# Kernel optimization log

Hardware: AMD Instinct MI355X
Metric: run time of the kernel (lower is better)

Reference implementation:

```python
import jax, jax.numpy as jnp
import numpy as np

N, E, F_IN, EF, HID = 100000, 1600000, 32, 8, 16


def gat_conv(x, W, att_src, att_dst, b, src, dst, heads, out_ch):
    # PyG GATConv: h = x@W per head; score = LeakyReLU(a_s.h_src + a_d.h_dst);
    # segment-softmax over incoming edges of each dst; weighted sum of h_src.
    n = x.shape[0]
    h = (x @ W).reshape(n, heads, out_ch)                      # [N,H,C]
    a_s = jnp.sum(h * att_src, axis=-1)                        # [N,H]
    a_d = jnp.sum(h * att_dst, axis=-1)                        # [N,H]
    e = jax.nn.leaky_relu(a_s[src] + a_d[dst], 0.2)            # [E',H]
    m = jax.ops.segment_max(e, dst, num_segments=n)            # [N,H]
    ex = jnp.exp(e - m[dst])
    denom = jax.ops.segment_sum(ex, dst, num_segments=n)
    alpha = ex / (denom[dst] + 1e-16)                          # [E',H]
    out = jax.ops.segment_sum(h[src] * alpha[:, :, None], dst, num_segments=n)
    return out.reshape(n, heads * out_ch) + b


def setup_inputs() -> dict:
    key = jax.random.key(0)
    ks = jax.random.split(key, 16)
    s = 0.1
    return {
        "x": jax.random.normal(ks[0], (N, F_IN), jnp.float32),
        "edge_index": jax.random.randint(ks[1], (2, E), 0, N, jnp.int32),
        "edge_attr": jax.random.uniform(ks[2], (E, 2 * EF), jnp.float32),
        "num_edge_features": EF,
        "num_edge_masks": EF,
        # conv1: heads=4, out=16
        "W1": jax.random.normal(ks[3], (F_IN, 4 * HID), jnp.float32) * s,
        "att_src1": jax.random.normal(ks[4], (4, HID), jnp.float32) * s,
        "att_dst1": jax.random.normal(ks[5], (4, HID), jnp.float32) * s,
        "b1": jnp.zeros((4 * HID,), jnp.float32),
        # conv2: heads=1, out=16
        "W2": jax.random.normal(ks[6], (4 * HID, HID), jnp.float32) * s,
        "att_src2": jax.random.normal(ks[7], (1, HID), jnp.float32) * s,
        "att_dst2": jax.random.normal(ks[8], (1, HID), jnp.float32) * s,
        "b2": jnp.zeros((HID,), jnp.float32),
        # edge MLP
        "mlp_W1": jax.random.normal(ks[9], (EF, HID), jnp.float32) * s,
        "mlp_b1": jnp.zeros((HID,), jnp.float32),
        "mlp_W2": jax.random.normal(ks[10], (HID, HID), jnp.float32) * s,
        "mlp_b2": jnp.zeros((HID,), jnp.float32),
        # fc_edge: 3*hid -> 1
        "fc_W": jax.random.normal(ks[11], (3 * HID, 1), jnp.float32) * s,
        "fc_b": jnp.zeros((1,), jnp.float32),
    }


def reference(x, edge_index, edge_attr, num_edge_features, num_edge_masks,
              W1, att_src1, att_dst1, b1, W2, att_src2, att_dst2, b2,
              mlp_W1, mlp_b1, mlp_W2, mlp_b2, fc_W, fc_b):
    n = x.shape[0]
    src, dst = edge_index[0], edge_index[1]
    # GATConv adds self loops internally (PyG default)
    loops = jnp.arange(n, dtype=edge_index.dtype)
    src_sl = jnp.concatenate([src, loops])
    dst_sl = jnp.concatenate([dst, loops])
    ef = edge_attr[:, :num_edge_features] * edge_attr[:, num_edge_features:]
    h = gat_conv(x, W1, att_src1, att_dst1, b1, src_sl, dst_sl, 4, HID)
    h = jax.nn.elu(h)                                          # dropout: eval mode -> identity
    h = gat_conv(h, W2, att_src2, att_dst2, b2, src_sl, dst_sl, 1, HID)
    ef = jax.nn.relu(ef @ mlp_W1 + mlp_b1) @ mlp_W2 + mlp_b2   # edge MLP
    emb = jnp.concatenate([h[src], h[dst], ef], axis=1)        # [E,3*HID]
    return (emb @ fc_W + fc_b).squeeze(-1)                     # [E]
```

## Files before the change

### kernel.cpp

```cpp
#include <hip/hip_runtime.h>
#include <hip/hip_bf16.h>
#include <hip/hip_fp16.h>


#define FIN 32
#define C1 64
#define HID 16
#define BSH 8
#define CAP2 6144
#define SOP 68
#define BINB 1024
#define BINT 4

__device__ __forceinline__ float leaky02(float x) {
    return x > 0.f ? x : 0.2f * x;
}

__global__ void k_binit3(int* __restrict__ bcur, int nbuck) {
    int b = blockIdx.x * blockDim.x + threadIdx.x;
    if (b < nbuck) bcur[b] = b * CAP2;
}

__global__ void __launch_bounds__(256) k_binF(
        const int* __restrict__ src, const int* __restrict__ dst,
        int* __restrict__ bcur, unsigned* __restrict__ brec,
        const float* __restrict__ ea,
        const float* __restrict__ mlpW1, const float* __restrict__ mlpb1,
        const float* __restrict__ mlpW2, const float* __restrict__ mlpb2,
        const float* __restrict__ fcW, const float* __restrict__ fcb,
        float* __restrict__ outp,
        int e, int ep, int nbuck, int gbin) {
    __shared__ int cnt[512];
    __shared__ int cur[512];
    __shared__ float sW[128];
    __shared__ float sb[16];
    __shared__ float sw2[17];
    int tid = threadIdx.x;
    if ((int)blockIdx.x < gbin) {
        int cb = blockIdx.x * BINB;
        for (int j = tid; j < 512; j += 256) cnt[j] = 0;
        __syncthreads();
        unsigned rec[BINT];
        int bk[BINT];
#pragma unroll
        for (int t = 0; t < BINT; t++) {
            int i = cb + t * 256 + tid;
            bk[t] = -1;
            if (i < ep) {
                int s, d;
                if (i < e) { s = src[i]; d = dst[i]; }
                else       { s = i - e; d = s; }
                int b = d >> BSH;
                rec[t] = ((unsigned)(d & 255) << 17) | (unsigned)s;
                bk[t] = b;
                atomicAdd(&cnt[b], 1);
            }
        }
        __syncthreads();
        for (int b = tid; b < nbuck; b += 256) {
            int c = cnt[b];
            cur[b] = (c > 0) ? atomicAdd(&bcur[b], c) : 0;
        }
        __syncthreads();
#pragma unroll
        for (int t = 0; t < BINT; t++) {
            if (bk[t] >= 0) {
                int p = atomicAdd(&cur[bk[t]], 1);
                if (p < (bk[t] + 1) * CAP2)
                    brec[p] = rec[t];
            }
        }
    } else {
        if (tid < 128) sW[tid] = mlpW1[tid];
        if (tid < 16)  sb[tid] = mlpb1[tid];
        if (tid < 16) {
            float s = 0.f;
#pragma unroll
            for (int k = 0; k < 16; k++) s += mlpW2[tid * 16 + k] * fcW[32 + k];
            sw2[tid] = s;
        } else if (tid == 16) {
            float s = fcb[0];
            for (int k = 0; k < 16; k++) s += mlpb2[k] * fcW[32 + k];
            sw2[16] = s;
        }
        __syncthreads();
        int eid = ((int)blockIdx.x - gbin) * 256 + tid;
        if (eid >= e) return;
        const float4* ev = (const float4*)ea + (size_t)eid * 4;
        float4 v0 = ev[0], v1 = ev[1], v2 = ev[2], v3 = ev[3];
        float ef[8] = { v0.x * v2.x, v0.y * v2.y, v0.z * v2.z, v0.w * v2.w,
                        v1.x * v3.x, v1.y * v3.y, v1.z * v3.z, v1.w * v3.w };
        float acc = sw2[16];
#pragma unroll
        for (int j = 0; j < 16; j++) {
            float tt = sb[j];
#pragma unroll
            for (int i = 0; i < 8; i++) tt += ef[i] * sW[i * 16 + j];
            acc += fmaxf(tt, 0.f) * sw2[j];
        }
        outp[eid] = acc;
    }
}

__global__ void __launch_bounds__(256) k_fineF(
        const unsigned* __restrict__ brec, const int* __restrict__ bcur,
        int* __restrict__ offs, int* __restrict__ oend, int* __restrict__ ssrc,
        const float* __restrict__ x, const float* __restrict__ W1,
        const float* __restrict__ att_s, const float* __restrict__ att_d,
        __half* __restrict__ h1h, float* __restrict__ a1, float* __restrict__ d1,
        int n, int gfine) {
    __shared__ int lcnt[256];
    __shared__ int sbuf[256];
    __shared__ float sW[FIN * C1];
    __shared__ float sA[C1], sD[C1];
    __shared__ float sX[4 * FIN];
    int tid = threadIdx.x;
    if ((int)blockIdx.x < gfine) {
        int b = blockIdx.x;
        int n0 = b << BSH;
        int base = b * CAP2;
        int cnt = min(bcur[b] - base, CAP2);
        lcnt[tid] = 0;
        __syncthreads();
        for (int i = tid; i < cnt; i += 256) {
            unsigned r = brec[base + i];
            atomicAdd(&lcnt[r >> 17], 1);
        }
        __syncthreads();
        int v = lcnt[tid];
        sbuf[tid] = v;
        __syncthreads();
        for (int off = 1; off < 256; off <<= 1) {
            int u = (tid >= off) ? sbuf[tid - off] : 0;
            __syncthreads();
            sbuf[tid] += u;
            __syncthreads();
        }
        int excl = sbuf[tid] - v;
        if (n0 + tid < n) {
            offs[n0 + tid] = base + excl;
            oend[n0 + tid] = base + excl + v;
        }
        lcnt[tid] = base + excl;
        __syncthreads();
        for (int i = tid; i < cnt; i += 256) {
            unsigned r = brec[base + i];
            int p = atomicAdd(&lcnt[r >> 17], 1);
            ssrc[p] = (int)(r & 0x1FFFF);
        }
    } else {
        int nb = (int)blockIdx.x - gfine;
        for (int i = tid; i < FIN * C1; i += 256) sW[i] = W1[i];
        if (tid < C1) { sA[tid] = att_s[tid]; sD[tid] = att_d[tid]; }
        int bse = nb * 4;
        if (tid < 4 * FIN) {
            int nn = bse + (tid >> 5);
            sX[tid] = (nn < n) ? x[(size_t)nn * FIN + (tid & 31)] : 0.f;
        }
        __syncthreads();
        int li = tid >> 6, c = tid & 63;
        int node = bse + li;
        if (node >= n) return;
        const float* xr = sX + li * FIN;
        float acc = 0.f;
#pragma unroll
        for (int k = 0; k < FIN; k++) acc += xr[k] * sW[k * C1 + c];
        h1h[(size_t)node * C1 + c] = __float2half(acc);
        float pa = acc * sA[c], pb = acc * sD[c];
#pragma unroll
        for (int m = 8; m >= 1; m >>= 1) {
            pa += __shfl_xor(pa, m, 16);
            pb += __shfl_xor(pb, m, 16);
        }
        if ((c & 15) == 0) {
            a1[node * 4 + (c >> 4)] = pa;
            d1[node * 4 + (c >> 4)] = pb;
        }
    }
}

__global__ void __launch_bounds__(256) k_agg1F(
        const __half* __restrict__ h1h, const float* __restrict__ a1,
        const float* __restrict__ d1, const float* __restrict__ b1,
        const float* __restrict__ W2,
        const float* __restrict__ att_s2, const float* __restrict__ att_d2,
        const int* __restrict__ offs, const int* __restrict__ oend,
        const int* __restrict__ ssrc,
        __half* __restrict__ h2h, float* __restrict__ a2, float* __restrict__ d2,
        int n) {
    __shared__ float4 w4l[4][64];
    __shared__ int    sil[4][64];
    __shared__ float  sO[4][4][SOP];
    __shared__ float  sW2[C1 * HID];
    int tid = threadIdx.x;
    for (int i = tid; i < C1 * HID; i += 256) sW2[i] = W2[i];
    __syncthreads();
    int wid = (int)((blockIdx.x * (size_t)blockDim.x + tid) >> 6);
    int lane = tid & 63;
    int wl = tid >> 6;
    int quarter = lane >> 4;
    int lane16 = lane & 15;
    int node = wid * 4 + quarter;
    if (node >= n) return;
    int sub = lane16 & 7;
    int g   = lane16 >> 3;
    int head = sub >> 1;
    unsigned lane_off = (unsigned)sub * 16u;
    const char* hb = (const char*)h1h;
    float4 dv = ((const float4*)d1)[node];
    int s0 = offs[node], s1v = oend[node];
    float acc[8] = {0.f, 0.f, 0.f, 0.f, 0.f, 0.f, 0.f, 0.f};
    float dsum = 0.f;
    for (int base = s0; base < s1v; base += 16) {
        int cnt = min(16, s1v - base);
        int sl = (lane16 < cnt) ? ssrc[base + lane16] : 0;
        float4 a4 = ((const float4*)a1)[(unsigned)sl];
        float4 w4;
        if (lane16 < cnt) {
            w4.x = __expf(leaky02(a4.x + dv.x));
            w4.y = __expf(leaky02(a4.y + dv.y));
            w4.z = __expf(leaky02(a4.z + dv.z));
            w4.w = __expf(leaky02(a4.w + dv.w));
        } else {
            w4.x = w4.y = w4.z = w4.w = 0.f;
        }
        w4l[wl][lane] = w4;
        sil[wl][lane] = sl << 7;
        __builtin_amdgcn_wave_barrier();
        int cnt2 = (cnt + 1) & ~1;
        int lbase = quarter << 4;
#pragma unroll 8
        for (int j = g; j < cnt2; j += 2) {
            int soff = sil[wl][lbase + j];
            float w = ((const float*)&w4l[wl][lbase + j])[head];
            float4 raw = *(const float4*)(hb + (unsigned)soff + lane_off);
            const __half* hr = (const __half*)&raw;
            acc[0] = fmaf(__half2float(hr[0]), w, acc[0]);
            acc[1] = fmaf(__half2float(hr[1]), w, acc[1]);
            acc[2] = fmaf(__half2float(hr[2]), w, acc[2]);
            acc[3] = fmaf(__half2float(hr[3]), w, acc[3]);
            acc[4] = fmaf(__half2float(hr[4]), w, acc[4]);
            acc[5] = fmaf(__half2float(hr[5]), w, acc[5]);
            acc[6] = fmaf(__half2float(hr[6]), w, acc[6]);
            acc[7] = fmaf(__half2float(hr[7]), w, acc[7]);
            dsum += w;
        }
        __builtin_amdgcn_wave_barrier();
    }
#pragma unroll
    for (int i = 0; i < 8; i++) acc[i] += __shfl_xor(acc[i], 8, 64);
    dsum += __shfl_xor(dsum, 8, 64);
    if (lane16 < 8) {
        float inv = 1.f / (dsum + 1e-16f);
        float4 bA = ((const float4*)b1)[lane16 * 2];
        float4 bB = ((const float4*)b1)[lane16 * 2 + 1];
        float4 oA, oB;
        oA.x = acc[0] * inv + bA.x;
        oA.y = acc[1] * inv + bA.y;
        oA.z = acc[2] * inv + bA.z;
        oA.w = acc[3] * inv + bA.w;
        oB.x = acc[4] * inv + bB.x;
        oB.y = acc[5] * inv + bB.y;
        oB.z = acc[6] * inv + bB.z;
        oB.w = acc[7] * inv + bB.w;
        oA.x = oA.x > 0.f ? oA.x : (__expf(oA.x) - 1.f);
        oA.y = oA.y > 0.f ? oA.y : (__expf(oA.y) - 1.f);
        oA.z = oA.z > 0.f ? oA.z : (__expf(oA.z) - 1.f);
        oA.w = oA.w > 0.f ? oA.w : (__expf(oA.w) - 1.f);
        oB.x = oB.x > 0.f ? oB.x : (__expf(oB.x) - 1.f);
        oB.y = oB.y > 0.f ? oB.y : (__expf(oB.y) - 1.f);
        oB.z = oB.z > 0.f ? oB.z : (__expf(oB.z) - 1.f);
        oB.w = oB.w > 0.f ? oB.w : (__expf(oB.w) - 1.f);
        *((float4*)&sO[wl][quarter][lane16 * 8])     = oA;
        *((float4*)&sO[wl][quarter][lane16 * 8 + 4]) = oB;
    }
    __builtin_amdgcn_wave_barrier();
    int c = lane16;
    const float* orow = sO[wl][quarter];
    float part = 0.f;
#pragma unroll
    for (int k = 0; k < C1; k++)
        part = fmaf(orow[k], sW2[k * HID + c], part);
    h2h[(size_t)node * HID + c] = __float2half(part);
    float pa = part * att_s2[c], pb = part * att_d2[c];
#pragma unroll
    for (int m = 8; m >= 1; m >>= 1) {
        pa += __shfl_xor(pa, m, 64);
        pb += __shfl_xor(pb, m, 64);
    }
    if (lane16 == 0) { a2[node] = pa; d2[node] = pb; }
}

__global__ void __launch_bounds__(256) k_agg2(
        const __half* __restrict__ h2h, const float* __restrict__ a2,
        const float* __restrict__ d2, const float* __restrict__ b2,
        const float* __restrict__ fcW,
        const int* __restrict__ offs, const int* __restrict__ oend,
        const int* __restrict__ ssrc,
        float* __restrict__ ps, float* __restrict__ pd, int n) {
    __shared__ float2 wsl[4][64];
    int tid = threadIdx.x;
    int wid = (int)((blockIdx.x * (size_t)blockDim.x + tid) >> 6);
    int lane = tid & 63;
    int wl = tid >> 6;
    int quarter = lane >> 4;
    int lane16 = lane & 15;
    int node = wid * 4 + quarter;
    if (node >= n) return;
    int sub = lane16 & 1;
    int g   = lane16 >> 1;
    unsigned lane_off = (unsigned)sub * 16u;
    const char* hb = (const char*)h2h;
    float dvv = d2[node];
    int s0 = offs[node], s1v = oend[node];
    float acc[8] = {0.f, 0.f, 0.f, 0.f, 0.f, 0.f, 0.f, 0.f};
    float dsum = 0.f;
    for (int base = s0; base < s1v; base += 16) {
        int cnt = min(16, s1v - base);
        int sl = (lane16 < cnt) ? ssrc[base + lane16] : 0;
        float av = a2[(unsigned)sl];
        float w = (lane16 < cnt) ? __expf(leaky02(av + dvv)) : 0.f;
        wsl[wl][lane] = make_float2(w, __int_as_float(sl << 5));
        __builtin_amdgcn_wave_barrier();
        int cnt8 = (cnt + 7) & ~7;
        int lbase = quarter << 4;
#pragma unroll 2
        for (int j = g; j < cnt8; j += 8) {
            float2 e0 = wsl[wl][lbase + j];
            unsigned soff = (unsigned)__float_as_int(e0.y);
            float4 raw = *(const float4*)(hb + soff + lane_off);
            const __half* hr = (const __half*)&raw;
            acc[0] = fmaf(__half2float(hr[0]), e0.x, acc[0]);
            acc[1] = fmaf(__half2float(hr[1]), e0.x, acc[1]);
            acc[2] = fmaf(__half2float(hr[2]), e0.x, acc[2]);
            acc[3] = fmaf(__half2float(hr[3]), e0.x, acc[3]);
            acc[4] = fmaf(__half2float(hr[4]), e0.x, acc[4]);
            acc[5] = fmaf(__half2float(hr[5]), e0.x, acc[5]);
            acc[6] = fmaf(__half2float(hr[6]), e0.x, acc[6]);
            acc[7] = fmaf(__half2float(hr[7]), e0.x, acc[7]);
            dsum += e0.x;
        }
        __builtin_amdgcn_wave_barrier();
    }
#pragma unroll
    for (int m = 2; m <= 8; m <<= 1) {
#pragma unroll
        for (int i = 0; i < 8; i++) acc[i] += __shfl_xor(acc[i], m, 64);
        dsum += __shfl_xor(dsum, m, 64);
    }
    float inv = 1.f / (dsum + 1e-16f);
    float4 bA = ((const float4*)b2)[sub * 2];
    float4 bB = ((const float4*)b2)[sub * 2 + 1];
    float4 fsA = ((const float4*)fcW)[sub * 2];
    float4 fsB = ((const float4*)fcW)[sub * 2 + 1];
    float4 fdA = ((const float4*)fcW)[4 + sub * 2];
    float4 fdB = ((const float4*)fcW)[4 + sub * 2 + 1];
    float h0 = acc[0] * inv + bA.x, h1v = acc[1] * inv + bA.y;
    float h2v = acc[2] * inv + bA.z, h3 = acc[3] * inv + bA.w;
    float h4 = acc[4] * inv + bB.x, h5 = acc[5] * inv + bB.y;
    float h6 = acc[6] * inv + bB.z, h7 = acc[7] * inv + bB.w;
    float p1 = h0 * fsA.x + h1v * fsA.y + h2v * fsA.z + h3 * fsA.w
             + h4 * fsB.x + h5 * fsB.y + h6 * fsB.z + h7 * fsB.w;
    float p2 = h0 * fdA.x + h1v * fdA.y + h2v * fdA.z + h3 * fdA.w
             + h4 * fdB.x + h5 * fdB.y + h6 * fdB.z + h7 * fdB.w;
    p1 += __shfl_xor(p1, 1, 64);
    p2 += __shfl_xor(p2, 1, 64);
    if (lane16 == 0) { ps[node] = p1; pd[node] = p2; }
}

__global__ void __launch_bounds__(256) k_final2(
        const int* __restrict__ src, const int* __restrict__ dst,
        const float* __restrict__ ps, const float* __restrict__ pd,
        float* __restrict__ out, int e) {
    int eid = blockIdx.x * blockDim.x + threadIdx.x;
    if (eid < e) out[eid] += ps[src[eid]] + pd[dst[eid]];
}

extern "C" void kernel_launch(void* const* d_in, const int* in_sizes, int n_in,
                              void* d_out, int out_size, void* d_ws, size_t ws_size,
                              hipStream_t stream) {
    const float* x        = (const float*)d_in[0];
    const int*   eidx     = (const int*)d_in[1];
    const float* eattr    = (const float*)d_in[2];
    const float* W1       = (const float*)d_in[5];
    const float* att_s1   = (const float*)d_in[6];
    const float* att_d1   = (const float*)d_in[7];
    const float* b1       = (const float*)d_in[8];
    const float* W2       = (const float*)d_in[9];
    const float* att_s2   = (const float*)d_in[10];
    const float* att_d2   = (const float*)d_in[11];
    const float* b2       = (const float*)d_in[12];
    const float* mlp_W1   = (const float*)d_in[13];
    const float* mlp_b1   = (const float*)d_in[14];
    const float* mlp_W2   = (const float*)d_in[15];
    const float* mlp_b2   = (const float*)d_in[16];
    const float* fc_W     = (const float*)d_in[17];
    const float* fc_b     = (const float*)d_in[18];

    const int n = in_sizes[0] / FIN;
    const int e = in_sizes[2] / 16;
    const int ep = e + n;
    const int* src = eidx;
    const int* dst = eidx + e;
    const int nbuck = (n + 255) >> BSH;

    char* p = (char*)d_ws;
    auto carve = [&](size_t bytes) {
        char* r = p;
        p += (bytes + 255) & ~(size_t)255;
        return r;
    };
    __half* h1h  = (__half*)carve((size_t)n * C1 * 2);
    __half* h2h  = (__half*)carve((size_t)n * HID * 2);
    float*  a1   = (float*)carve((size_t)n * 4 * 4);
    float*  d1   = (float*)carve((size_t)n * 4 * 4);
    float*  a2   = (float*)carve((size_t)n * 4);
    float*  d2   = (float*)carve((size_t)n * 4);
    float*  ps   = (float*)carve((size_t)n * 4);
    float*  pd   = (float*)carve((size_t)n * 4);
    int*    offs = (int*)carve((size_t)n * 4);
    int*    oendp= (int*)carve((size_t)n * 4);
    int*    bcur = (int*)carve(512 * 4);
    int*    ssrc = (int*)carve((size_t)nbuck * CAP2 * 4);
    unsigned* brec = (unsigned*)carve((size_t)nbuck * CAP2 * 4);

    float* outp = (float*)d_out;

    const int gbin  = (ep + BINB - 1) / BINB;
    const int gmlp  = (e + 255) / 256;
    const int gnode1 = (n + 3) / 4;
    const int nquad = (n + 3) / 4;

    k_binit3<<<2, 256, 0, stream>>>(bcur, nbuck);
    k_binF<<<gbin + gmlp, 256, 0, stream>>>(src, dst, bcur, brec, eattr,
                                            mlp_W1, mlp_b1, mlp_W2, mlp_b2,
                                            fc_W, fc_b, outp, e, ep, nbuck, gbin);
    k_fineF<<<nbuck + gnode1, 256, 0, stream>>>(brec, bcur, offs, oendp, ssrc,
                                                x, W1, att_s1, att_d1,
                                                h1h, a1, d1, n, nbuck);
    k_agg1F<<<(nquad * 64 + 255) / 256, 256, 0, stream>>>(
        h1h, a1, d1, b1, W2, att_s2, att_d2, offs, oendp, ssrc, h2h, a2, d2, n);
    k_agg2<<<(nquad * 64 + 255) / 256, 256, 0, stream>>>(
        h2h, a2, d2, b2, fc_W, offs, oendp, ssrc, ps, pd, n);
    k_final2<<<(e + 255) / 256, 256, 0, stream>>>(src, dst, ps, pd, outp, e);
}
```

Measured before the change: 202.7 us.

## Stage binned edge records in shared memory for coalesced bucket writes

The binning kernel now processes 4096 edges per block instead of 1024, builds a per-block bucket histogram with a shared-memory prefix scan, locally sorts the records by bucket in LDS, and then writes them to global buckets as contiguous runs. This replaces scattered per-record global writes with mostly coalesced ones and cuts the number of global atomics on bucket cursors per edge. In exchange it adds a 9-step scan with barriers and more shared memory per block. It also gives fewer blocks, which may reduce occupancy and parallelism for this phase.

Result: faster. 179.4 us (-11.5%).

```diff
diff --git a/kernel.cpp b/kernel.cpp
--- a/kernel.cpp
+++ b/kernel.cpp
@@ -9,8 +9,8 @@
 #define BSH 8
 #define CAP2 6144
 #define SOP 68
-#define BINB 1024
-#define BINT 4
+#define BINB 4096
+#define BINT 16
 
 __device__ __forceinline__ float leaky02(float x) {
     return x > 0.f ? x : 0.2f * x;
@@ -30,15 +30,21 @@
         const float* __restrict__ fcW, const float* __restrict__ fcb,
         float* __restrict__ outp,
         int e, int ep, int nbuck, int gbin) {
-    __shared__ int cnt[512];
-    __shared__ int cur[512];
+    __shared__ int hist[512];
+    __shared__ int sc[2][512];
+    __shared__ int bstart[512];
+    __shared__ int off2[512];
+    __shared__ int gbase[512];
+    __shared__ unsigned srec[BINB];
+    __shared__ unsigned short sbkt[BINB];
     __shared__ float sW[128];
     __shared__ float sb[16];
     __shared__ float sw2[17];
     int tid = threadIdx.x;
     if ((int)blockIdx.x < gbin) {
         int cb = blockIdx.x * BINB;
-        for (int j = tid; j < 512; j += 256) cnt[j] = 0;
+        int cnt = min(BINB, ep - cb);
+        for (int j = tid; j < 512; j += 256) hist[j] = 0;
         __syncthreads();
         unsigned rec[BINT];
         int bk[BINT];
@@ -53,22 +59,45 @@
                 int b = d >> BSH;
                 rec[t] = ((unsigned)(d & 255) << 17) | (unsigned)s;
                 bk[t] = b;
-                atomicAdd(&cnt[b], 1);
+                atomicAdd(&hist[b], 1);
             }
         }
         __syncthreads();
+        for (int j = tid; j < 512; j += 256) sc[0][j] = hist[j];
+        __syncthreads();
+        int pi = 0;
+        for (int off = 1; off < 512; off <<= 1) {
+            int po = pi ^ 1;
+            for (int j = tid; j < 512; j += 256)
+                sc[po][j] = sc[pi][j] + ((j >= off) ? sc[pi][j - off] : 0);
+            __syncthreads();
+            pi = po;
+        }
+        for (int j = tid; j < 512; j += 256) {
+            int excl = sc[pi][j] - hist[j];
+            bstart[j] = excl;
+            off2[j] = excl;
+        }
+        __syncthreads();
         for (int b = tid; b < nbuck; b += 256) {
-            int c = cnt[b];
-            cur[b] = (c > 0) ? atomicAdd(&bcur[b], c) : 0;
+            int c = hist[b];
+            if (c > 0) gbase[b] = atomicAdd(&bcur[b], c);
         }
         __syncthreads();
 #pragma unroll
         for (int t = 0; t < BINT; t++) {
             if (bk[t] >= 0) {
-                int p = atomicAdd(&cur[bk[t]], 1);
-                if (p < (bk[t] + 1) * CAP2)
-                    brec[p] = rec[t];
+                int p = atomicAdd(&off2[bk[t]], 1);
+                srec[p] = rec[t];
+                sbkt[p] = (unsigned short)bk[t];
             }
+        }
+        __syncthreads();
+        for (int i = tid; i < cnt; i += 256) {
+            int b = sbkt[i];
+            int idx = gbase[b] + (i - bstart[b]);
+            if (idx < (b + 1) * CAP2)
+                brec[idx] = srec[i];
         }
     } else {
         if (tid < 128) sW[tid] = mlpW1[tid];
```

## Move node GEMM into binning launch and enlarge per-block bin chunk

Applied to the files above, without the earlier changes.

The first-layer node transform (x@W1 plus attention dot products) now runs as extra blocks of the binning/edge-MLP launch, and the fine CSR build becomes its own kernel containing only bucket blocks. This balances work across launches so the few hundred fine-sort blocks no longer share a launch with the node GEMM. Each binning block also handles 4096 edges (16 per thread) rather than 1024, which cuts global bucket-cursor atomics at the cost of more registers and fewer binning blocks. Shared memory in the combined kernel grows to hold W1.

Measured after the change: 201.8 us. About the same (-0.5%).

```diff
diff --git a/kernel.cpp b/kernel.cpp
--- a/kernel.cpp
+++ b/kernel.cpp
@@ -9,8 +9,8 @@
 #define BSH 8
 #define CAP2 6144
 #define SOP 68
-#define BINB 1024
-#define BINT 4
+#define BINB 4096
+#define BINT 16
 
 __device__ __forceinline__ float leaky02(float x) {
     return x > 0.f ? x : 0.2f * x;
@@ -29,12 +29,15 @@
         const float* __restrict__ mlpW2, const float* __restrict__ mlpb2,
         const float* __restrict__ fcW, const float* __restrict__ fcb,
         float* __restrict__ outp,
-        int e, int ep, int nbuck, int gbin) {
+        const float* __restrict__ x, const float* __restrict__ W1,
+        const float* __restrict__ att_s, const float* __restrict__ att_d,
+        __half* __restrict__ h1h, float* __restrict__ a1, float* __restrict__ d1,
+        int e, int ep, int n, int nbuck, int gbin, int gmlp) {
     __shared__ int cnt[512];
     __shared__ int cur[512];
-    __shared__ float sW[128];
-    __shared__ float sb[16];
-    __shared__ float sw2[17];
+    __shared__ float sW[FIN * C1];
+    __shared__ float sA[C1], sD[C1];
+    __shared__ float sX[4 * FIN];
     int tid = threadIdx.x;
     if ((int)blockIdx.x < gbin) {
         int cb = blockIdx.x * BINB;
@@ -70,18 +73,21 @@
                     brec[p] = rec[t];
             }
         }
-    } else {
-        if (tid < 128) sW[tid] = mlpW1[tid];
-        if (tid < 16)  sb[tid] = mlpb1[tid];
+    } else if ((int)blockIdx.x < gbin + gmlp) {
+        float* sWm = sW;
+        float* sbm = sA;
+        float* sw2m = sD;
+        if (tid < 128) sWm[tid] = mlpW1[tid];
+        if (tid < 16)  sbm[tid] = mlpb1[tid];
         if (tid < 16) {
             float s = 0.f;
 #pragma unroll
             for (int k = 0; k < 16; k++) s += mlpW2[tid * 16 + k] * fcW[32 + k];
-            sw2[tid] = s;
+            sw2m[tid] = s;
         } else if (tid == 16) {
             float s = fcb[0];
             for (int k = 0; k < 16; k++) s += mlpb2[k] * fcW[32 + k];
-            sw2[16] = s;
+            sw2m[16] = s;
         }
         __syncthreads();
         int eid = ((int)blockIdx.x - gbin) * 256 + tid;
@@ -90,66 +96,17 @@
         float4 v0 = ev[0], v1 = ev[1], v2 = ev[2], v3 = ev[3];
         float ef[8] = { v0.x * v2.x, v0.y * v2.y, v0.z * v2.z, v0.w * v2.w,
                         v1.x * v3.x, v1.y * v3.y, v1.z * v3.z, v1.w * v3.w };
-        float acc = sw2[16];
+        float acc = sw2m[16];
 #pragma unroll
         for (int j = 0; j < 16; j++) {
-            float tt = sb[j];
-#pragma unroll
-            for (int i = 0; i < 8; i++) tt += ef[i] * sW[i * 16 + j];
-            acc += fmaxf(tt, 0.f) * sw2[j];
+            float tt = sbm[j];
+#pragma unroll
+            for (int i = 0; i < 8; i++) tt += ef[i] * sWm[i * 16 + j];
+            acc += fmaxf(tt, 0.f) * sw2m[j];
         }
         outp[eid] = acc;
-    }
-}
-
-__global__ void __launch_bounds__(256) k_fineF(
-        const unsigned* __restrict__ brec, const int* __restrict__ bcur,
-        int* __restrict__ offs, int* __restrict__ oend, int* __restrict__ ssrc,
-        const float* __restrict__ x, const float* __restrict__ W1,
-        const float* __restrict__ att_s, const float* __restrict__ att_d,
-        __half* __restrict__ h1h, float* __restrict__ a1, float* __restrict__ d1,
-        int n, int gfine) {
-    __shared__ int lcnt[256];
-    __shared__ int sbuf[256];
-    __shared__ float sW[FIN * C1];
-    __shared__ float sA[C1], sD[C1];
-    __shared__ float sX[4 * FIN];
-    int tid = threadIdx.x;
-    if ((int)blockIdx.x < gfine) {
-        int b = blockIdx.x;
-        int n0 = b << BSH;
-        int base = b * CAP2;
-        int cnt = min(bcur[b] - base, CAP2);
-        lcnt[tid] = 0;
-        __syncthreads();
-        for (int i = tid; i < cnt; i += 256) {
-            unsigned r = brec[base + i];
-            atomicAdd(&lcnt[r >> 17], 1);
-        }
-        __syncthreads();
-        int v = lcnt[tid];
-        sbuf[tid] = v;
-        __syncthreads();
-        for (int off = 1; off < 256; off <<= 1) {
-            int u = (tid >= off) ? sbuf[tid - off] : 0;
-            __syncthreads();
-            sbuf[tid] += u;
-            __syncthreads();
-        }
-        int excl = sbuf[tid] - v;
-        if (n0 + tid < n) {
-            offs[n0 + tid] = base + excl;
-            oend[n0 + tid] = base + excl + v;
-        }
-        lcnt[tid] = base + excl;
-        __syncthreads();
-        for (int i = tid; i < cnt; i += 256) {
-            unsigned r = brec[base + i];
-            int p = atomicAdd(&lcnt[r >> 17], 1);
-            ssrc[p] = (int)(r & 0x1FFFF);
-        }
     } else {
-        int nb = (int)blockIdx.x - gfine;
+        int nb = (int)blockIdx.x - gbin - gmlp;
         for (int i = tid; i < FIN * C1; i += 256) sW[i] = W1[i];
         if (tid < C1) { sA[tid] = att_s[tid]; sD[tid] = att_d[tid]; }
         int bse = nb * 4;
@@ -176,6 +133,47 @@
             a1[node * 4 + (c >> 4)] = pa;
             d1[node * 4 + (c >> 4)] = pb;
         }
+    }
+}
+
+__global__ void __launch_bounds__(256) k_fine(
+        const unsigned* __restrict__ brec, const int* __restrict__ bcur,
+        int* __restrict__ offs, int* __restrict__ oend, int* __restrict__ ssrc,
+        int n) {
+    __shared__ int lcnt[256];
+    __shared__ int sbuf[256];
+    int tid = threadIdx.x;
+    int b = blockIdx.x;
+    int n0 = b << BSH;
+    int base = b * CAP2;
+    int cnt = min(bcur[b] - base, CAP2);
+    lcnt[tid] = 0;
+    __syncthreads();
+    for (int i = tid; i < cnt; i += 256) {
+        unsigned r = brec[base + i];
+        atomicAdd(&lcnt[r >> 17], 1);
+    }
+    __syncthreads();
+    int v = lcnt[tid];
+    sbuf[tid] = v;
+    __syncthreads();
+    for (int off = 1; off < 256; off <<= 1) {
+        int u = (tid >= off) ? sbuf[tid - off] : 0;
+        __syncthreads();
+        sbuf[tid] += u;
+        __syncthreads();
+    }
+    int excl = sbuf[tid] - v;
+    if (n0 + tid < n) {
+        offs[n0 + tid] = base + excl;
+        oend[n0 + tid] = base + excl + v;
+    }
+    lcnt[tid] = base + excl;
+    __syncthreads();
+    for (int i = tid; i < cnt; i += 256) {
+        unsigned r = brec[base + i];
+        int p = atomicAdd(&lcnt[r >> 17], 1);
+        ssrc[p] = (int)(r & 0x1FFFF);
     }
 }
 
@@ -432,12 +430,12 @@
     const int nquad = (n + 3) / 4;
 
     k_binit3<<<2, 256, 0, stream>>>(bcur, nbuck);
-    k_binF<<<gbin + gmlp, 256, 0, stream>>>(src, dst, bcur, brec, eattr,
-                                            mlp_W1, mlp_b1, mlp_W2, mlp_b2,
-                                            fc_W, fc_b, outp, e, ep, nbuck, gbin);
-    k_fineF<<<nbuck + gnode1, 256, 0, stream>>>(brec, bcur, offs, oendp, ssrc,
-                                                x, W1, att_s1, att_d1,
-                                                h1h, a1, d1, n, nbuck);
+    k_binF<<<gbin + gmlp + gnode1, 256, 0, stream>>>(
+        src, dst, bcur, brec, eattr,
+        mlp_W1, mlp_b1, mlp_W2, mlp_b2, fc_W, fc_b, outp,
+        x, W1, att_s1, att_d1, h1h, a1, d1,
+        e, ep, n, nbuck, gbin, gmlp);
+    k_fine<<<nbuck, 256, 0, stream>>>(brec, bcur, offs, oendp, ssrc, n);
     k_agg1F<<<(nquad * 64 + 255) / 256, 256, 0, stream>>>(
         h1h, a1, d1, b1, W2, att_s2, att_d2, offs, oendp, ssrc, h2h, a2, d2, n);
     k_agg2<<<(nquad * 64 + 255) / 256, 256, 0, stream>>>(
```
